# Kernel tuning notes

Hardware: AMD Instinct MI355X
Metric: run time of the kernel (lower is better)

The kernel has to match this reference:

```python
import jax, jax.numpy as jnp
import numpy as np

B, Q, C = 16, 2048, 256
SCORE_THRESH = 0.05   # lowered from 0.7 so the mask is non-trivial with 256 classes
NMS_THRESH = 0.7
LABEL_OFFSET = 1e5    # batched_nms trick: offset boxes per class so cross-class IoU ~ 0


def box_cxcywh_to_xyxy(b):
    cx, cy, w, h = jnp.split(b, 4, axis=-1)
    return jnp.concatenate([cx - 0.5 * w, cy - 0.5 * h, cx + 0.5 * w, cy + 0.5 * h], axis=-1)


def pairwise_iou(boxes):
    # boxes: [N,4] xyxy -> iou: [N,N]
    area = jnp.clip(boxes[:, 2] - boxes[:, 0], 0) * jnp.clip(boxes[:, 3] - boxes[:, 1], 0)
    lt = jnp.maximum(boxes[:, None, :2], boxes[None, :, :2])
    rb = jnp.minimum(boxes[:, None, 2:], boxes[None, :, 2:])
    wh = jnp.clip(rb - lt, 0)
    inter = wh[..., 0] * wh[..., 1]
    union = area[:, None] + area[None, :] - inter
    return inter / jnp.maximum(union, 1e-6)


def nms_single(boxes, scores, labels, valid):
    # Emulates torchvision batched_nms with fixed-size (padded) output:
    # returns score-sorted boxes/scores/labels plus a boolean keep mask.
    n = boxes.shape[0]
    boxes_off = boxes + labels.astype(boxes.dtype)[:, None] * LABEL_OFFSET
    order = jnp.argsort(jnp.where(valid, scores, -jnp.inf))[::-1]
    b_off = boxes_off[order]
    s = scores[order]
    l = labels[order]
    v = valid[order]
    iou = pairwise_iou(b_off)  # [N,N], class-offset so only same-class overlap
    idx = jnp.arange(n)

    def step(keep, x):
        row, i = x  # row: iou of box i vs all
        sup = (row > NMS_THRESH) & (idx > i) & keep[i]
        return keep & ~sup, None

    keep, _ = jax.lax.scan(step, v, (iou, idx))
    return boxes[order], s, l, keep & v


def setup_inputs() -> dict:
    key = jax.random.key(0)
    k1, k2, k3 = jax.random.split(key, 3)
    pred_logits = jax.random.normal(k1, (B, Q, C), dtype=jnp.float32)
    pred_boxes = jax.random.uniform(k2, (B, Q, 4), dtype=jnp.float32)
    target_sizes = jax.random.randint(k3, (B, 2), 480, 1333, dtype=jnp.int32)
    return {"pred_logits": pred_logits, "pred_boxes": pred_boxes, "target_sizes": target_sizes}


def reference(pred_logits, pred_boxes, target_sizes):
    prob = jax.nn.softmax(pred_logits, axis=-1)
    cls_prob = prob[..., :-1]            # drop 'no-object' class
    scores = cls_prob.max(axis=-1)       # [B,Q]
    labels = cls_prob.argmax(axis=-1)    # [B,Q]
    boxes = box_cxcywh_to_xyxy(pred_boxes)
    ts = target_sizes.astype(boxes.dtype)
    img_h, img_w = ts[:, 0], ts[:, 1]
    scale = jnp.stack([img_w, img_h, img_w, img_h], axis=1)  # [B,4]
    boxes = boxes * scale[:, None, :]
    valid = scores >= SCORE_THRESH
    out_boxes, out_scores, out_labels, keep = jax.vmap(nms_single)(boxes, scores, labels, valid)
    return out_boxes, out_scores, out_labels, keep
```

## Files before the change

kernel.cpp:

```cpp
#include <hip/hip_runtime.h>
#include <math.h>

#define NB 16
#define BQ 2048
#define NC 256
#define NL 255

typedef unsigned long long u64;
typedef unsigned int u32;
typedef unsigned short u16;
typedef unsigned char u8;

__device__ __forceinline__ u32 ord_f32(float f) {
  u32 b = __float_as_uint(f);
  return (b & 0x80000000u) ? ~b : (b | 0x80000000u);
}

__global__ __launch_bounds__(256) void score_box_kernel(
    const float* __restrict__ logits,
    const float* __restrict__ pboxes,
    const int* __restrict__ tsz,
    float* __restrict__ out)
{
#pragma clang fp contract(off)
  const int lane = threadIdx.x & 63;
  const int g = lane & 15;
  const int wv = threadIdx.x >> 6;
  const int q = (blockIdx.x * 4 + wv) * 4 + (lane >> 4);
  const float* row = logits + (size_t)q * NC + g * 16;
  const float4 la = *reinterpret_cast<const float4*>(row);
  const float4 lb4 = *reinterpret_cast<const float4*>(row + 4);
  const float4 lc = *reinterpret_cast<const float4*>(row + 8);
  const float4 ld = *reinterpret_cast<const float4*>(row + 12);

  float m = fmaxf(fmaxf(fmaxf(la.x, la.y), fmaxf(la.z, la.w)),
           fmaxf(fmaxf(fmaxf(lb4.x, lb4.y), fmaxf(lb4.z, lb4.w)),
           fmaxf(fmaxf(fmaxf(lc.x, lc.y), fmaxf(lc.z, lc.w)),
                 fmaxf(fmaxf(ld.x, ld.y), fmaxf(ld.z, ld.w)))));
  #pragma unroll
  for (int d = 1; d < 16; d <<= 1) m = fmaxf(m, __shfl_xor(m, d));

  float4 ea, eb, ec, ed;
  ea.x = expf(la.x - m);  ea.y = expf(la.y - m);  ea.z = expf(la.z - m);  ea.w = expf(la.w - m);
  eb.x = expf(lb4.x - m); eb.y = expf(lb4.y - m); eb.z = expf(lb4.z - m); eb.w = expf(lb4.w - m);
  ec.x = expf(lc.x - m);  ec.y = expf(lc.y - m);  ec.z = expf(lc.z - m);  ec.w = expf(lc.w - m);
  ed.x = expf(ld.x - m);  ed.y = expf(ld.y - m);  ed.z = expf(ld.z - m);  ed.w = expf(ld.w - m);

  float s = (((ea.x + ea.y) + (ea.z + ea.w)) + ((eb.x + eb.y) + (eb.z + eb.w)))
          + (((ec.x + ec.y) + (ec.z + ec.w)) + ((ed.x + ed.y) + (ed.z + ed.w)));
  #pragma unroll
  for (int d = 1; d < 16; d <<= 1) s += __shfl_xor(s, d);

  const int c0 = g * 16;
  float bp = ea.x / s; int bc = c0;
  float p;
  p = ea.y / s; if (p > bp) { bp = p; bc = c0 + 1; }
  p = ea.z / s; if (p > bp) { bp = p; bc = c0 + 2; }
  p = ea.w / s; if (p > bp) { bp = p; bc = c0 + 3; }
  p = eb.x / s; if (p > bp) { bp = p; bc = c0 + 4; }
  p = eb.y / s; if (p > bp) { bp = p; bc = c0 + 5; }
  p = eb.z / s; if (p > bp) { bp = p; bc = c0 + 6; }
  p = eb.w / s; if (p > bp) { bp = p; bc = c0 + 7; }
  p = ec.x / s; if (p > bp) { bp = p; bc = c0 + 8; }
  p = ec.y / s; if (p > bp) { bp = p; bc = c0 + 9; }
  p = ec.z / s; if (p > bp) { bp = p; bc = c0 + 10; }
  p = ec.w / s; if (p > bp) { bp = p; bc = c0 + 11; }
  p = ed.x / s; if (p > bp) { bp = p; bc = c0 + 12; }
  p = ed.y / s; if (p > bp) { bp = p; bc = c0 + 13; }
  p = ed.z / s; if (p > bp) { bp = p; bc = c0 + 14; }
  p = ed.w / s; if (g != 15 && p > bp) { bp = p; bc = c0 + 15; }
  #pragma unroll
  for (int d = 1; d < 16; d <<= 1) {
    const float op = __shfl_xor(bp, d);
    const int   oc = __shfl_xor(bc, d);
    if (op > bp || (op == bp && oc < bc)) { bp = op; bc = oc; }
  }

  if (g == 0) {
    const int b = q >> 11;
    float hf = (float)tsz[b * 2 + 0];
    float wf = (float)tsz[b * 2 + 1];
    float4 pb = *reinterpret_cast<const float4*>(pboxes + (size_t)q * 4);
    float hw = 0.5f * pb.z, hh = 0.5f * pb.w;
    float4 ob;
    ob.x = (pb.x - hw) * wf;
    ob.y = (pb.y - hh) * hf;
    ob.z = (pb.x + hw) * wf;
    ob.w = (pb.y + hh) * hf;
    *reinterpret_cast<float4*>(out + (size_t)q * 4) = ob;
    out[NB * BQ * 4 + q] = bp;
    out[NB * BQ * 5 + q] = (float)bc;
  }
}

__global__ __launch_bounds__(1024) void sort_nms_kernel(float* __restrict__ out)
{
#pragma clang fp contract(off)
  __shared__ __align__(16) u64 cvk[BQ];
  __shared__ u32 cgt_a[BQ];
  __shared__ float4 bx[BQ];
  __shared__ float4 bxo[BQ];
  __shared__ u16 gposu[NL * 64];
  __shared__ u8 lbp[BQ];
  __shared__ u8 grank[BQ];
  __shared__ u32 kcnt[256];
  __shared__ u32 wval[16], winv[16];

  const int b = blockIdx.x;
  const int tid = threadIdx.x;
  const int lane = tid & 63;
  const int wv = tid >> 6;
  float* boxes_g  = out + (size_t)b * BQ * 4;
  float* scores_g = out + NB * BQ * 4 + (size_t)b * BQ;
  float* labels_g = out + NB * BQ * 5 + (size_t)b * BQ;
  float* keep_g   = out + NB * BQ * 6 + (size_t)b * BQ;

  const int q0 = 2 * tid;
  float2 s2 = *reinterpret_cast<const float2*>(scores_g + q0);
  float2 lf = *reinterpret_cast<const float2*>(labels_g + q0);
  float4 bb0 = *reinterpret_cast<const float4*>(boxes_g + (size_t)q0 * 4);
  float4 bb1 = *reinterpret_cast<const float4*>(boxes_g + (size_t)q0 * 4 + 4);
  const u32 l0 = (u32)(int)lf.x, l1 = (u32)(int)lf.y;
  bx[q0] = bb0; bx[q0 + 1] = bb1;
  cgt_a[tid] = 0; cgt_a[tid + 1024] = 0;
  if (tid < 256) kcnt[tid] = 0;
  const bool v0 = (s2.x >= 0.05f), v1 = (s2.y >= 0.05f);
  const u64 f0 = ((u64)ord_f32(s2.x) << 32) | ((u32)q0 << 8) | l0;
  const u64 f1 = ((u64)ord_f32(s2.y) << 32) | ((u32)(q0 + 1) << 8) | l1;
  const u64 b0 = __ballot(v0), b1 = __ballot(v1);
  if (lane == 0) {
    const u32 c = (u32)(__popcll(b0) + __popcll(b1));
    wval[wv] = c;
    winv[wv] = 128u - c;
  }
  __syncthreads();

  int nv = 0, voff = 0, ioff = 0;
  #pragma unroll
  for (int w = 0; w < 16; ++w) {
    const int c = (int)wval[w];
    nv += c;
    if (w < wv) { voff += c; ioff += (int)winv[w]; }
  }
  const int tinv = BQ - nv;
  const u64 below = (1ull << lane) - 1ull;
  const int vr0 = voff + (int)__popcll(b0 & below) + (int)__popcll(b1 & below);
  const int ir0 = ioff + (int)__popcll(~b0 & below) + (int)__popcll(~b1 & below);
  const int vr1 = vr0 + (v0 ? 1 : 0);
  const int ir1 = ir0 + (v0 ? 0 : 1);
  if (v0) cvk[vr0] = f0;
  else {
    const int ip = nv + (tinv - 1 - ir0);
    *reinterpret_cast<float4*>(boxes_g + (size_t)ip * 4) = bb0;
    scores_g[ip] = s2.x; labels_g[ip] = lf.x; keep_g[ip] = 0.0f;
  }
  if (v1) cvk[vr1] = f1;
  else {
    const int ip = nv + (tinv - 1 - ir1);
    *reinterpret_cast<float4*>(boxes_g + (size_t)ip * 4) = bb1;
    scores_g[ip] = s2.y; labels_g[ip] = lf.y; keep_g[ip] = 0.0f;
  }
  const int nvc = (nv + 63) >> 6;
  for (int pp = nv + tid; pp < (nvc << 6); pp += 1024) cvk[pp] = 0;
  __syncthreads();

  {
    const int nvS = (nv + 255) >> 8;
    const int nitems = nvS * nvc;
    for (int it = wv; it < nitems; it += 16) {
      const int sc_ = it / nvc;
      const int jc = it - sc_ * nvc;
      const int sb = (sc_ << 8) + lane;
      const u64 ki0 = cvk[sb];
      const u64 ki1 = cvk[sb + 64];
      const u64 ki2 = cvk[sb + 128];
      const u64 ki3 = cvk[sb + 192];
      const ulonglong2* jp2 = reinterpret_cast<const ulonglong2*>(&cvk[jc << 6]);
      u32 c0 = 0, c1 = 0, c2 = 0, c3 = 0;
      #pragma unroll 4
      for (int l2 = 0; l2 < 32; ++l2) {
        const ulonglong2 kj = jp2[l2];
        c0 += ((kj.x > ki0) ? 1u : 0u) + ((kj.y > ki0) ? 1u : 0u);
        c1 += ((kj.x > ki1) ? 1u : 0u) + ((kj.y > ki1) ? 1u : 0u);
        c2 += ((kj.x > ki2) ? 1u : 0u) + ((kj.y > ki2) ? 1u : 0u);
        c3 += ((kj.x > ki3) ? 1u : 0u) + ((kj.y > ki3) ? 1u : 0u);
      }
      if (sb < nv && c0)       atomicAdd(&cgt_a[sb], c0);
      if (sb + 64 < nv && c1)  atomicAdd(&cgt_a[sb + 64], c1);
      if (sb + 128 < nv && c2) atomicAdd(&cgt_a[sb + 128], c2);
      if (sb + 192 < nv && c3) atomicAdd(&cgt_a[sb + 192], c3);
    }
  }
  __syncthreads();

  for (int slot = tid; slot < nv; slot += 1024) {
    const u64 ki = cvk[slot];
    const u32 p = cgt_a[slot];
    const u32 oi = (u32)(ki >> 8) & (BQ - 1);
    const u32 li = (u32)ki & 255u;
    const float4 A = bx[oi];
    *reinterpret_cast<float4*>(boxes_g + (size_t)p * 4) = A;
    scores_g[p] = __uint_as_float((u32)(ki >> 32) & 0x7FFFFFFFu);
    labels_g[p] = (float)li;
    lbp[p] = (u8)li;
    const float lc = (float)li * 100000.0f;
    float4 Ao;
    Ao.x = A.x + lc; Ao.y = A.y + lc; Ao.z = A.z + lc; Ao.w = A.w + lc;
    bxo[p] = Ao;
    const u32 arr = atomicAdd(&kcnt[li], 1u);
    if (arr < 64) gposu[li * 64 + arr] = (u16)p;
  }
  __syncthreads();

  if (tid < NL) {
    const int l = tid;
    int k = (int)kcnt[l]; if (k > 64) k = 64;
    const int base = l * 64;
    for (int a = 1; a < k; ++a) {
      const u16 v = gposu[base + a];
      int e = a;
      while (e > 0 && gposu[base + e - 1] > v) { gposu[base + e] = gposu[base + e - 1]; --e; }
      gposu[base + e] = v;
    }
    if ((int)kcnt[l] <= 64)
      for (int r = 0; r < k; ++r) grank[gposu[base + r]] = (u8)r;
  }
  __syncthreads();

  for (int p = tid; p < nv; p += 1024) {
    const u32 li = lbp[p];
    if (kcnt[li] <= 64) {
      const u32 g = grank[p];
      const u32 st = li * 64;
      const float4 Ao = bxo[p];
      const float areaA = fmaxf(Ao.z - Ao.x, 0.0f) * fmaxf(Ao.w - Ao.y, 0.0f);
      u64 m = 0;
      for (u32 r = 0; r < g; ++r) {
        const int p2 = gposu[st + r];
        const float4 Bo = bxo[p2];
        const float areaB = fmaxf(Bo.z - Bo.x, 0.0f) * fmaxf(Bo.w - Bo.y, 0.0f);
        const float ltx = fmaxf(Ao.x, Bo.x), lty = fmaxf(Ao.y, Bo.y);
        const float rbx = fminf(Ao.z, Bo.z), rby = fminf(Ao.w, Bo.w);
        const float iw = fmaxf(rbx - ltx, 0.0f), ih = fmaxf(rby - lty, 0.0f);
        const float inter = iw * ih;
        const float uni = (areaA + areaB) - inter;
        const float iou = inter / fmaxf(uni, 1e-6f);
        if (iou > 0.7f) m |= (1ull << r);
      }
      cvk[p] = m;
    }
  }
  __syncthreads();

  if (tid < NL) {
    const int l = tid;
    const int k = (int)kcnt[l];
    if (k > 0 && k <= 64) {
      const int st = l * 64;
      u64 kept = 0;
      for (int r = 0; r < k; ++r) {
        const u16 pr = gposu[st + r];
        const u64 m = cvk[pr];
        const int keep = ((m & kept) == 0) ? 1 : 0;
        kept |= (u64)keep << r;
        keep_g[pr] = keep ? 1.0f : 0.0f;
      }
    } else if (k > 64) {
      for (int p2 = 0; p2 < nv; ++p2) {
        if ((int)lbp[p2] != l) continue;
        const float4 Ao = bxo[p2];
        const float areaA = fmaxf(Ao.z - Ao.x, 0.0f) * fmaxf(Ao.w - Ao.y, 0.0f);
        int keep = 1;
        for (int e = 0; e < p2; ++e) {
          if ((int)lbp[e] != l || !grank[e]) continue;
          const float4 Bo = bxo[e];
          const float areaB = fmaxf(Bo.z - Bo.x, 0.0f) * fmaxf(Bo.w - Bo.y, 0.0f);
          const float ltx = fmaxf(Ao.x, Bo.x), lty = fmaxf(Ao.y, Bo.y);
          const float rbx = fminf(Ao.z, Bo.z), rby = fminf(Ao.w, Bo.w);
          const float iw = fmaxf(rbx - ltx, 0.0f), ih = fmaxf(rby - lty, 0.0f);
          const float inter = iw * ih;
          const float uni = (areaA + areaB) - inter;
          const float iou = inter / fmaxf(uni, 1e-6f);
          if (iou > 0.7f) { keep = 0; break; }
        }
        grank[p2] = (u8)keep;
        keep_g[p2] = keep ? 1.0f : 0.0f;
      }
    }
  }
}

extern "C" void kernel_launch(void* const* d_in, const int* in_sizes, int n_in,
                              void* d_out, int out_size, void* d_ws, size_t ws_size,
                              hipStream_t stream) {
  const float* logits = (const float*)d_in[0];
  const float* pboxes = (const float*)d_in[1];
  const int*   tsz    = (const int*)d_in[2];
  float* out = (float*)d_out;
  score_box_kernel<<<NB * BQ / 16, 256, 0, stream>>>(logits, pboxes, tsz, out);
  sort_nms_kernel<<<NB, 1024, 0, stream>>>(out);
}
```

Baseline: 30.66 us.

## Split sort+NMS into compact, multi-block rank, and finish kernels

Splits the single per-image sort/NMS kernel into three launches. A compact kernel writes the valid keys to workspace. A rank kernel then computes counting-sort ranks using 8 blocks per image instead of 16 waves in one block. A finish kernel does the scatter and NMS, staging outputs in shared memory before writing them out coalesced. This spreads the O(n^2) rank work across more CUs, at the cost of two extra launches and global-memory round trips; the rank kernel also reads keys from global memory in a scalar loop.

```diff
diff --git a/kernel.cpp b/kernel.cpp
--- a/kernel.cpp
+++ b/kernel.cpp
@@ -20,7 +20,7 @@
     const float* __restrict__ logits,
     const float* __restrict__ pboxes,
     const int* __restrict__ tsz,
-    float* __restrict__ out)
+    float* __restrict__ ws)
 {
 #pragma clang fp contract(off)
   const int lane = threadIdx.x & 63;
@@ -87,43 +87,39 @@
     ob.y = (pb.y - hh) * hf;
     ob.z = (pb.x + hw) * wf;
     ob.w = (pb.y + hh) * hf;
-    *reinterpret_cast<float4*>(out + (size_t)q * 4) = ob;
-    out[NB * BQ * 4 + q] = bp;
-    out[NB * BQ * 5 + q] = (float)bc;
-  }
-}
-
-__global__ __launch_bounds__(1024) void sort_nms_kernel(float* __restrict__ out)
+    *reinterpret_cast<float4*>(ws + (size_t)q * 4) = ob;
+    ws[NB * BQ * 4 + q] = bp;
+    ws[NB * BQ * 5 + q] = (float)bc;
+  }
+}
+
+__global__ __launch_bounds__(1024) void compact_kernel(
+    const float* __restrict__ ws, float* __restrict__ out,
+    u64* __restrict__ keys_g, u32* __restrict__ nv_g)
 {
-#pragma clang fp contract(off)
   __shared__ __align__(16) u64 cvk[BQ];
-  __shared__ u32 cgt_a[BQ];
-  __shared__ float4 bx[BQ];
-  __shared__ float4 bxo[BQ];
-  __shared__ u16 gposu[NL * 64];
-  __shared__ u8 lbp[BQ];
-  __shared__ u8 grank[BQ];
-  __shared__ u32 kcnt[256];
   __shared__ u32 wval[16], winv[16];
 
   const int b = blockIdx.x;
   const int tid = threadIdx.x;
   const int lane = tid & 63;
   const int wv = tid >> 6;
+  const float* sws = ws + NB * BQ * 4 + (size_t)b * BQ;
+  const float* lws = ws + NB * BQ * 5 + (size_t)b * BQ;
+  const float* bws = ws + (size_t)b * BQ * 4;
   float* boxes_g  = out + (size_t)b * BQ * 4;
   float* scores_g = out + NB * BQ * 4 + (size_t)b * BQ;
   float* labels_g = out + NB * BQ * 5 + (size_t)b * BQ;
   float* keep_g   = out + NB * BQ * 6 + (size_t)b * BQ;
 
   const int q0 = 2 * tid;
-  float2 s2 = *reinterpret_cast<const float2*>(scores_g + q0);
-  float2 lf = *reinterpret_cast<const float2*>(labels_g + q0);
-  float4 bb0 = *reinterpret_cast<const float4*>(boxes_g + (size_t)q0 * 4);
-  float4 bb1 = *reinterpret_cast<const float4*>(boxes_g + (size_t)q0 * 4 + 4);
+  float2 s2 = *reinterpret_cast<const float2*>(sws + q0);
+  float2 lf = *reinterpret_cast<const float2*>(lws + q0);
   const u32 l0 = (u32)(int)lf.x, l1 = (u32)(int)lf.y;
-  bx[q0] = bb0; bx[q0 + 1] = bb1;
-  cgt_a[tid] = 0; cgt_a[tid + 1024] = 0;
-  if (tid < 256) kcnt[tid] = 0;
+  {
+    ulonglong2 z; z.x = 0; z.y = 0;
+    *reinterpret_cast<ulonglong2*>(&cvk[q0]) = z;
+  }
   const bool v0 = (s2.x >= 0.05f), v1 = (s2.y >= 0.05f);
   const u64 f0 = ((u64)ord_f32(s2.x) << 32) | ((u32)q0 << 8) | l0;
   const u64 f1 = ((u64)ord_f32(s2.y) << 32) | ((u32)(q0 + 1) << 8) | l1;
@@ -151,59 +147,92 @@
   if (v0) cvk[vr0] = f0;
   else {
     const int ip = nv + (tinv - 1 - ir0);
-    *reinterpret_cast<float4*>(boxes_g + (size_t)ip * 4) = bb0;
+    *reinterpret_cast<float4*>(boxes_g + (size_t)ip * 4) =
+        *reinterpret_cast<const float4*>(bws + (size_t)q0 * 4);
     scores_g[ip] = s2.x; labels_g[ip] = lf.x; keep_g[ip] = 0.0f;
   }
   if (v1) cvk[vr1] = f1;
   else {
     const int ip = nv + (tinv - 1 - ir1);
-    *reinterpret_cast<float4*>(boxes_g + (size_t)ip * 4) = bb1;
+    *reinterpret_cast<float4*>(boxes_g + (size_t)ip * 4) =
+        *reinterpret_cast<const float4*>(bws + (size_t)q0 * 4 + 4);
     scores_g[ip] = s2.y; labels_g[ip] = lf.y; keep_g[ip] = 0.0f;
   }
-  const int nvc = (nv + 63) >> 6;
-  for (int pp = nv + tid; pp < (nvc << 6); pp += 1024) cvk[pp] = 0;
   __syncthreads();
 
   {
-    const int nvS = (nv + 255) >> 8;
-    const int nitems = nvS * nvc;
-    for (int it = wv; it < nitems; it += 16) {
-      const int sc_ = it / nvc;
-      const int jc = it - sc_ * nvc;
-      const int sb = (sc_ << 8) + lane;
-      const u64 ki0 = cvk[sb];
-      const u64 ki1 = cvk[sb + 64];
-      const u64 ki2 = cvk[sb + 128];
-      const u64 ki3 = cvk[sb + 192];
-      const ulonglong2* jp2 = reinterpret_cast<const ulonglong2*>(&cvk[jc << 6]);
-      u32 c0 = 0, c1 = 0, c2 = 0, c3 = 0;
-      #pragma unroll 4
-      for (int l2 = 0; l2 < 32; ++l2) {
-        const ulonglong2 kj = jp2[l2];
-        c0 += ((kj.x > ki0) ? 1u : 0u) + ((kj.y > ki0) ? 1u : 0u);
-        c1 += ((kj.x > ki1) ? 1u : 0u) + ((kj.y > ki1) ? 1u : 0u);
-        c2 += ((kj.x > ki2) ? 1u : 0u) + ((kj.y > ki2) ? 1u : 0u);
-        c3 += ((kj.x > ki3) ? 1u : 0u) + ((kj.y > ki3) ? 1u : 0u);
-      }
-      if (sb < nv && c0)       atomicAdd(&cgt_a[sb], c0);
-      if (sb + 64 < nv && c1)  atomicAdd(&cgt_a[sb + 64], c1);
-      if (sb + 128 < nv && c2) atomicAdd(&cgt_a[sb + 128], c2);
-      if (sb + 192 < nv && c3) atomicAdd(&cgt_a[sb + 192], c3);
-    }
-  }
+    u64* kb = keys_g + (size_t)b * BQ;
+    *reinterpret_cast<ulonglong2*>(&kb[q0]) =
+        *reinterpret_cast<const ulonglong2*>(&cvk[q0]);
+  }
+  if (tid == 0) nv_g[b] = (u32)nv;
+}
+
+__global__ __launch_bounds__(256) void rank_kernel(
+    const u64* __restrict__ keys_g, const u32* __restrict__ nv_g,
+    u32* __restrict__ rnk_g)
+{
+  const int b = blockIdx.x >> 3;
+  const int slice = blockIdx.x & 7;
+  const int tid = threadIdx.x;
+  const int nv = (int)nv_g[b];
+  const int slot = slice * 256 + tid;
+  if (slice * 256 >= nv) return;
+  const int nvp = (nv + 63) & ~63;
+  const u64* kb = keys_g + (size_t)b * BQ;
+  const u64 ki = kb[slot];
+  u32 c = 0;
+  #pragma unroll 8
+  for (int j = 0; j < nvp; ++j) c += (kb[j] > ki) ? 1u : 0u;
+  if (slot < nv) rnk_g[(size_t)b * BQ + slot] = c;
+}
+
+__global__ __launch_bounds__(1024) void finish_kernel(
+    const float* __restrict__ ws, const u64* __restrict__ keys_g,
+    const u32* __restrict__ nv_g, const u32* __restrict__ rnk_g,
+    float* __restrict__ out)
+{
+#pragma clang fp contract(off)
+  __shared__ __align__(16) u64 cvk[BQ];
+  __shared__ float4 bx[BQ];
+  __shared__ float4 bxo[BQ];
+  __shared__ u16 gposu[NL * 64];
+  __shared__ u16 sidx[BQ];
+  __shared__ u32 sco[BQ];
+  __shared__ u8 lbp[BQ];
+  __shared__ u8 grank[BQ];
+  __shared__ u8 kpf[BQ];
+  __shared__ u32 kcnt[256];
+
+  const int b = blockIdx.x;
+  const int tid = threadIdx.x;
+  const int nv = (int)nv_g[b];
+  const float* bws = ws + (size_t)b * BQ * 4;
+  const u64* kb = keys_g + (size_t)b * BQ;
+  const u32* rb = rnk_g + (size_t)b * BQ;
+  float* boxes_g  = out + (size_t)b * BQ * 4;
+  float* scores_g = out + NB * BQ * 4 + (size_t)b * BQ;
+  float* labels_g = out + NB * BQ * 5 + (size_t)b * BQ;
+  float* keep_g   = out + NB * BQ * 6 + (size_t)b * BQ;
+
+  const int q0 = 2 * tid;
+  *reinterpret_cast<ulonglong2*>(&cvk[q0]) =
+      *reinterpret_cast<const ulonglong2*>(&kb[q0]);
+  bx[q0]     = *reinterpret_cast<const float4*>(bws + (size_t)q0 * 4);
+  bx[q0 + 1] = *reinterpret_cast<const float4*>(bws + (size_t)q0 * 4 + 4);
+  if (tid < 256) kcnt[tid] = 0;
   __syncthreads();
 
   for (int slot = tid; slot < nv; slot += 1024) {
     const u64 ki = cvk[slot];
-    const u32 p = cgt_a[slot];
+    const u32 p = rb[slot];
     const u32 oi = (u32)(ki >> 8) & (BQ - 1);
     const u32 li = (u32)ki & 255u;
+    sidx[p] = (u16)oi;
+    lbp[p] = (u8)li;
+    sco[p] = (u32)(ki >> 32) & 0x7FFFFFFFu;
+    const float lc = (float)li * 100000.0f;
     const float4 A = bx[oi];
-    *reinterpret_cast<float4*>(boxes_g + (size_t)p * 4) = A;
-    scores_g[p] = __uint_as_float((u32)(ki >> 32) & 0x7FFFFFFFu);
-    labels_g[p] = (float)li;
-    lbp[p] = (u8)li;
-    const float lc = (float)li * 100000.0f;
     float4 Ao;
     Ao.x = A.x + lc; Ao.y = A.y + lc; Ao.z = A.z + lc; Ao.w = A.w + lc;
     bxo[p] = Ao;
@@ -263,7 +292,7 @@
         const u64 m = cvk[pr];
         const int keep = ((m & kept) == 0) ? 1 : 0;
         kept |= (u64)keep << r;
-        keep_g[pr] = keep ? 1.0f : 0.0f;
+        kpf[pr] = (u8)keep;
       }
     } else if (k > 64) {
       for (int p2 = 0; p2 < nv; ++p2) {
@@ -284,9 +313,17 @@
           if (iou > 0.7f) { keep = 0; break; }
         }
         grank[p2] = (u8)keep;
-        keep_g[p2] = keep ? 1.0f : 0.0f;
+        kpf[p2] = (u8)keep;
       }
     }
+  }
+  __syncthreads();
+
+  for (int p = tid; p < nv; p += 1024) {
+    *reinterpret_cast<float4*>(boxes_g + (size_t)p * 4) = bx[sidx[p]];
+    scores_g[p] = __uint_as_float(sco[p]);
+    labels_g[p] = (float)lbp[p];
+    keep_g[p]   = kpf[p] ? 1.0f : 0.0f;
   }
 }
 
@@ -297,6 +334,13 @@
   const float* pboxes = (const float*)d_in[1];
   const int*   tsz    = (const int*)d_in[2];
   float* out = (float*)d_out;
-  score_box_kernel<<<NB * BQ / 16, 256, 0, stream>>>(logits, pboxes, tsz, out);
-  sort_nms_kernel<<<NB, 1024, 0, stream>>>(out);
-}
+  float* ws  = (float*)d_ws;
+  char* wsb = (char*)d_ws;
+  u64* keys_g = (u64*)(wsb + (size_t)NB * BQ * 6 * 4);
+  u32* rnk_g  = (u32*)(wsb + (size_t)NB * BQ * 6 * 4 + (size_t)NB * BQ * 8);
+  u32* nv_g   = (u32*)(wsb + (size_t)NB * BQ * 6 * 4 + (size_t)NB * BQ * 8 + (size_t)NB * BQ * 4);
+  score_box_kernel<<<NB * BQ / 16, 256, 0, stream>>>(logits, pboxes, tsz, ws);
+  compact_kernel<<<NB, 1024, 0, stream>>>(ws, out, keys_g, nv_g);
+  rank_kernel<<<NB * 8, 256, 0, stream>>>(keys_g, nv_g, rnk_g);
+  finish_kernel<<<NB, 1024, 0, stream>>>(ws, keys_g, nv_g, rnk_g, out);
+}
```

Result: slower. 51.78 us (+68.9%).

## Split sort/NMS kernel across two blocks per image by label half

Applied to the files above, without the earlier changes.

Launches two blocks per image instead of one. Each block repeats the score sort, then builds per-label groups and runs NMS only for its half of the 255 labels. This halves per-block shared memory for the label tables and spreads the serial per-label NMS work over twice as many CUs, at the cost of doing the rank-counting sort twice. Both blocks read the image's data from the output buffer and write sorted results back into that same buffer with no ordering between blocks, so a block that starts late could read entries the other block has already overwritten.

```diff
diff --git a/kernel.cpp b/kernel.cpp
--- a/kernel.cpp
+++ b/kernel.cpp
@@ -100,13 +100,15 @@
   __shared__ u32 cgt_a[BQ];
   __shared__ float4 bx[BQ];
   __shared__ float4 bxo[BQ];
-  __shared__ u16 gposu[NL * 64];
+  __shared__ u16 gposu[128 * 64];
   __shared__ u8 lbp[BQ];
   __shared__ u8 grank[BQ];
-  __shared__ u32 kcnt[256];
+  __shared__ u32 kcnt[128];
   __shared__ u32 wval[16], winv[16];
 
-  const int b = blockIdx.x;
+  const int b = blockIdx.x >> 1;
+  const int h = blockIdx.x & 1;
+  const u32 labLo = (u32)h * 128u;
   const int tid = threadIdx.x;
   const int lane = tid & 63;
   const int wv = tid >> 6;
@@ -123,7 +125,8 @@
   const u32 l0 = (u32)(int)lf.x, l1 = (u32)(int)lf.y;
   bx[q0] = bb0; bx[q0 + 1] = bb1;
   cgt_a[tid] = 0; cgt_a[tid + 1024] = 0;
-  if (tid < 256) kcnt[tid] = 0;
+  lbp[q0] = 255; lbp[q0 + 1] = 255;
+  if (tid < 128) kcnt[tid] = 0;
   const bool v0 = (s2.x >= 0.05f), v1 = (s2.y >= 0.05f);
   const u64 f0 = ((u64)ord_f32(s2.x) << 32) | ((u32)q0 << 8) | l0;
   const u64 f1 = ((u64)ord_f32(s2.y) << 32) | ((u32)(q0 + 1) << 8) | l1;
@@ -149,13 +152,13 @@
   const int vr1 = vr0 + (v0 ? 1 : 0);
   const int ir1 = ir0 + (v0 ? 0 : 1);
   if (v0) cvk[vr0] = f0;
-  else {
+  else if (h == 0) {
     const int ip = nv + (tinv - 1 - ir0);
     *reinterpret_cast<float4*>(boxes_g + (size_t)ip * 4) = bb0;
     scores_g[ip] = s2.x; labels_g[ip] = lf.x; keep_g[ip] = 0.0f;
   }
   if (v1) cvk[vr1] = f1;
-  else {
+  else if (h == 0) {
     const int ip = nv + (tinv - 1 - ir1);
     *reinterpret_cast<float4*>(boxes_g + (size_t)ip * 4) = bb1;
     scores_g[ip] = s2.y; labels_g[ip] = lf.y; keep_g[ip] = 0.0f;
@@ -195,43 +198,48 @@
 
   for (int slot = tid; slot < nv; slot += 1024) {
     const u64 ki = cvk[slot];
-    const u32 p = cgt_a[slot];
-    const u32 oi = (u32)(ki >> 8) & (BQ - 1);
     const u32 li = (u32)ki & 255u;
-    const float4 A = bx[oi];
-    *reinterpret_cast<float4*>(boxes_g + (size_t)p * 4) = A;
-    scores_g[p] = __uint_as_float((u32)(ki >> 32) & 0x7FFFFFFFu);
-    labels_g[p] = (float)li;
-    lbp[p] = (u8)li;
-    const float lc = (float)li * 100000.0f;
-    float4 Ao;
-    Ao.x = A.x + lc; Ao.y = A.y + lc; Ao.z = A.z + lc; Ao.w = A.w + lc;
-    bxo[p] = Ao;
-    const u32 arr = atomicAdd(&kcnt[li], 1u);
-    if (arr < 64) gposu[li * 64 + arr] = (u16)p;
-  }
-  __syncthreads();
-
-  if (tid < NL) {
-    const int l = tid;
-    int k = (int)kcnt[l]; if (k > 64) k = 64;
-    const int base = l * 64;
+    if ((li - labLo) < 128u) {
+      const u32 p = cgt_a[slot];
+      const u32 oi = (u32)(ki >> 8) & (BQ - 1);
+      const float4 A = bx[oi];
+      *reinterpret_cast<float4*>(boxes_g + (size_t)p * 4) = A;
+      scores_g[p] = __uint_as_float((u32)(ki >> 32) & 0x7FFFFFFFu);
+      labels_g[p] = (float)li;
+      lbp[p] = (u8)li;
+      const float lc = (float)li * 100000.0f;
+      float4 Ao;
+      Ao.x = A.x + lc; Ao.y = A.y + lc; Ao.z = A.z + lc; Ao.w = A.w + lc;
+      bxo[p] = Ao;
+      const u32 ll = li - labLo;
+      const u32 arr = atomicAdd(&kcnt[ll], 1u);
+      if (arr < 64) gposu[ll * 64 + arr] = (u16)p;
+    }
+  }
+  __syncthreads();
+
+  if (tid < 128) {
+    const int ll = tid;
+    int k = (int)kcnt[ll]; if (k > 64) k = 64;
+    const int base = ll * 64;
     for (int a = 1; a < k; ++a) {
       const u16 v = gposu[base + a];
       int e = a;
       while (e > 0 && gposu[base + e - 1] > v) { gposu[base + e] = gposu[base + e - 1]; --e; }
       gposu[base + e] = v;
     }
-    if ((int)kcnt[l] <= 64)
+    if ((int)kcnt[ll] <= 64)
       for (int r = 0; r < k; ++r) grank[gposu[base + r]] = (u8)r;
   }
   __syncthreads();
 
   for (int p = tid; p < nv; p += 1024) {
     const u32 li = lbp[p];
-    if (kcnt[li] <= 64) {
+    if (li == 255u) continue;
+    const u32 ll = li - labLo;
+    if (kcnt[ll] <= 64) {
       const u32 g = grank[p];
-      const u32 st = li * 64;
+      const u32 st = ll * 64;
       const float4 Ao = bxo[p];
       const float areaA = fmaxf(Ao.z - Ao.x, 0.0f) * fmaxf(Ao.w - Ao.y, 0.0f);
       u64 m = 0;
@@ -252,11 +260,12 @@
   }
   __syncthreads();
 
-  if (tid < NL) {
-    const int l = tid;
-    const int k = (int)kcnt[l];
+  if (tid < 128) {
+    const int ll = tid;
+    const int li = (int)labLo + ll;
+    const int k = (int)kcnt[ll];
     if (k > 0 && k <= 64) {
-      const int st = l * 64;
+      const int st = ll * 64;
       u64 kept = 0;
       for (int r = 0; r < k; ++r) {
         const u16 pr = gposu[st + r];
@@ -267,12 +276,12 @@
       }
     } else if (k > 64) {
       for (int p2 = 0; p2 < nv; ++p2) {
-        if ((int)lbp[p2] != l) continue;
+        if ((int)lbp[p2] != li) continue;
         const float4 Ao = bxo[p2];
         const float areaA = fmaxf(Ao.z - Ao.x, 0.0f) * fmaxf(Ao.w - Ao.y, 0.0f);
         int keep = 1;
         for (int e = 0; e < p2; ++e) {
-          if ((int)lbp[e] != l || !grank[e]) continue;
+          if ((int)lbp[e] != li || !grank[e]) continue;
           const float4 Bo = bxo[e];
           const float areaB = fmaxf(Bo.z - Bo.x, 0.0f) * fmaxf(Bo.w - Bo.y, 0.0f);
           const float ltx = fmaxf(Ao.x, Bo.x), lty = fmaxf(Ao.y, Bo.y);
@@ -298,5 +307,5 @@
   const int*   tsz    = (const int*)d_in[2];
   float* out = (float*)d_out;
   score_box_kernel<<<NB * BQ / 16, 256, 0, stream>>>(logits, pboxes, tsz, out);
-  sort_nms_kernel<<<NB, 1024, 0, stream>>>(out);
+  sort_nms_kernel<<<NB * 2, 1024, 0, stream>>>(out);
 }
```

Measured after the change: 31.16 us. About the same (+1.6%).

## Fuse score and NMS kernels into one launch with per-batch flag sync

Applied to the files above, without the earlier changes.

Merges the softmax/box kernel and the sort/NMS kernel into a single launch. The first 512 blocks compute scores into a workspace, and 16 trailing blocks spin on per-batch atomic counters before running NMS. This removes the second kernel launch and lets NMS for early batches overlap with scoring of later ones. In exchange it adds a memset launch, spin-wait cost, dynamic shared memory, and a reduced per-class group cap (32), which routes more classes to the slow fallback path; it also relies on producer blocks being scheduled before the consumers to avoid deadlock.

```diff
diff --git a/kernel.cpp b/kernel.cpp
--- a/kernel.cpp
+++ b/kernel.cpp
@@ -5,6 +5,8 @@
 #define BQ 2048
 #define NC 256
 #define NL 255
+#define ABLK 512
+#define GCAP 32
 
 typedef unsigned long long u64;
 typedef unsigned int u32;
@@ -16,112 +18,127 @@
   return (b & 0x80000000u) ? ~b : (b | 0x80000000u);
 }
 
-__global__ __launch_bounds__(256) void score_box_kernel(
+__global__ __launch_bounds__(1024, 8) void fused_kernel(
     const float* __restrict__ logits,
     const float* __restrict__ pboxes,
     const int* __restrict__ tsz,
+    float* __restrict__ ws,
+    u32* __restrict__ flag,
     float* __restrict__ out)
 {
 #pragma clang fp contract(off)
-  const int lane = threadIdx.x & 63;
-  const int g = lane & 15;
-  const int wv = threadIdx.x >> 6;
-  const int q = (blockIdx.x * 4 + wv) * 4 + (lane >> 4);
-  const float* row = logits + (size_t)q * NC + g * 16;
-  const float4 la = *reinterpret_cast<const float4*>(row);
-  const float4 lb4 = *reinterpret_cast<const float4*>(row + 4);
-  const float4 lc = *reinterpret_cast<const float4*>(row + 8);
-  const float4 ld = *reinterpret_cast<const float4*>(row + 12);
-
-  float m = fmaxf(fmaxf(fmaxf(la.x, la.y), fmaxf(la.z, la.w)),
-           fmaxf(fmaxf(fmaxf(lb4.x, lb4.y), fmaxf(lb4.z, lb4.w)),
-           fmaxf(fmaxf(fmaxf(lc.x, lc.y), fmaxf(lc.z, lc.w)),
-                 fmaxf(fmaxf(ld.x, ld.y), fmaxf(ld.z, ld.w)))));
-  #pragma unroll
-  for (int d = 1; d < 16; d <<= 1) m = fmaxf(m, __shfl_xor(m, d));
-
-  float4 ea, eb, ec, ed;
-  ea.x = expf(la.x - m);  ea.y = expf(la.y - m);  ea.z = expf(la.z - m);  ea.w = expf(la.w - m);
-  eb.x = expf(lb4.x - m); eb.y = expf(lb4.y - m); eb.z = expf(lb4.z - m); eb.w = expf(lb4.w - m);
-  ec.x = expf(lc.x - m);  ec.y = expf(lc.y - m);  ec.z = expf(lc.z - m);  ec.w = expf(lc.w - m);
-  ed.x = expf(ld.x - m);  ed.y = expf(ld.y - m);  ed.z = expf(ld.z - m);  ed.w = expf(ld.w - m);
-
-  float s = (((ea.x + ea.y) + (ea.z + ea.w)) + ((eb.x + eb.y) + (eb.z + eb.w)))
-          + (((ec.x + ec.y) + (ec.z + ec.w)) + ((ed.x + ed.y) + (ed.z + ed.w)));
-  #pragma unroll
-  for (int d = 1; d < 16; d <<= 1) s += __shfl_xor(s, d);
-
-  const int c0 = g * 16;
-  float bp = ea.x / s; int bc = c0;
-  float p;
-  p = ea.y / s; if (p > bp) { bp = p; bc = c0 + 1; }
-  p = ea.z / s; if (p > bp) { bp = p; bc = c0 + 2; }
-  p = ea.w / s; if (p > bp) { bp = p; bc = c0 + 3; }
-  p = eb.x / s; if (p > bp) { bp = p; bc = c0 + 4; }
-  p = eb.y / s; if (p > bp) { bp = p; bc = c0 + 5; }
-  p = eb.z / s; if (p > bp) { bp = p; bc = c0 + 6; }
-  p = eb.w / s; if (p > bp) { bp = p; bc = c0 + 7; }
-  p = ec.x / s; if (p > bp) { bp = p; bc = c0 + 8; }
-  p = ec.y / s; if (p > bp) { bp = p; bc = c0 + 9; }
-  p = ec.z / s; if (p > bp) { bp = p; bc = c0 + 10; }
-  p = ec.w / s; if (p > bp) { bp = p; bc = c0 + 11; }
-  p = ed.x / s; if (p > bp) { bp = p; bc = c0 + 12; }
-  p = ed.y / s; if (p > bp) { bp = p; bc = c0 + 13; }
-  p = ed.z / s; if (p > bp) { bp = p; bc = c0 + 14; }
-  p = ed.w / s; if (g != 15 && p > bp) { bp = p; bc = c0 + 15; }
-  #pragma unroll
-  for (int d = 1; d < 16; d <<= 1) {
-    const float op = __shfl_xor(bp, d);
-    const int   oc = __shfl_xor(bc, d);
-    if (op > bp || (op == bp && oc < bc)) { bp = op; bc = oc; }
-  }
-
-  if (g == 0) {
-    const int b = q >> 11;
-    float hf = (float)tsz[b * 2 + 0];
-    float wf = (float)tsz[b * 2 + 1];
-    float4 pb = *reinterpret_cast<const float4*>(pboxes + (size_t)q * 4);
-    float hw = 0.5f * pb.z, hh = 0.5f * pb.w;
-    float4 ob;
-    ob.x = (pb.x - hw) * wf;
-    ob.y = (pb.y - hh) * hf;
-    ob.z = (pb.x + hw) * wf;
-    ob.w = (pb.y + hh) * hf;
-    *reinterpret_cast<float4*>(out + (size_t)q * 4) = ob;
-    out[NB * BQ * 4 + q] = bp;
-    out[NB * BQ * 5 + q] = (float)bc;
-  }
-}
-
-__global__ __launch_bounds__(1024) void sort_nms_kernel(float* __restrict__ out)
-{
-#pragma clang fp contract(off)
-  __shared__ __align__(16) u64 cvk[BQ];
-  __shared__ u32 cgt_a[BQ];
-  __shared__ float4 bx[BQ];
-  __shared__ float4 bxo[BQ];
-  __shared__ u16 gposu[NL * 64];
-  __shared__ u8 lbp[BQ];
-  __shared__ u8 grank[BQ];
-  __shared__ u32 kcnt[256];
-  __shared__ u32 wval[16], winv[16];
-
-  const int b = blockIdx.x;
+  extern __shared__ __align__(16) char smem[];
   const int tid = threadIdx.x;
   const int lane = tid & 63;
+
+  if (blockIdx.x < ABLK) {
+    const int g = lane & 15;
+    const int wv6 = tid >> 6;
+    const int q = blockIdx.x * 64 + wv6 * 4 + (lane >> 4);
+    const float* row = logits + (size_t)q * NC + g * 16;
+    const float4 la = *reinterpret_cast<const float4*>(row);
+    const float4 lb4 = *reinterpret_cast<const float4*>(row + 4);
+    const float4 lc = *reinterpret_cast<const float4*>(row + 8);
+    const float4 ld = *reinterpret_cast<const float4*>(row + 12);
+
+    float m = fmaxf(fmaxf(fmaxf(la.x, la.y), fmaxf(la.z, la.w)),
+             fmaxf(fmaxf(fmaxf(lb4.x, lb4.y), fmaxf(lb4.z, lb4.w)),
+             fmaxf(fmaxf(fmaxf(lc.x, lc.y), fmaxf(lc.z, lc.w)),
+                   fmaxf(fmaxf(ld.x, ld.y), fmaxf(ld.z, ld.w)))));
+    #pragma unroll
+    for (int d = 1; d < 16; d <<= 1) m = fmaxf(m, __shfl_xor(m, d));
+
+    float4 ea, eb, ec, ed;
+    ea.x = expf(la.x - m);  ea.y = expf(la.y - m);  ea.z = expf(la.z - m);  ea.w = expf(la.w - m);
+    eb.x = expf(lb4.x - m); eb.y = expf(lb4.y - m); eb.z = expf(lb4.z - m); eb.w = expf(lb4.w - m);
+    ec.x = expf(lc.x - m);  ec.y = expf(lc.y - m);  ec.z = expf(lc.z - m);  ec.w = expf(lc.w - m);
+    ed.x = expf(ld.x - m);  ed.y = expf(ld.y - m);  ed.z = expf(ld.z - m);  ed.w = expf(ld.w - m);
+
+    float s = (((ea.x + ea.y) + (ea.z + ea.w)) + ((eb.x + eb.y) + (eb.z + eb.w)))
+            + (((ec.x + ec.y) + (ec.z + ec.w)) + ((ed.x + ed.y) + (ed.z + ed.w)));
+    #pragma unroll
+    for (int d = 1; d < 16; d <<= 1) s += __shfl_xor(s, d);
+
+    const int c0 = g * 16;
+    float bp = ea.x / s; int bc = c0;
+    float p;
+    p = ea.y / s; if (p > bp) { bp = p; bc = c0 + 1; }
+    p = ea.z / s; if (p > bp) { bp = p; bc = c0 + 2; }
+    p = ea.w / s; if (p > bp) { bp = p; bc = c0 + 3; }
+    p = eb.x / s; if (p > bp) { bp = p; bc = c0 + 4; }
+    p = eb.y / s; if (p > bp) { bp = p; bc = c0 + 5; }
+    p = eb.z / s; if (p > bp) { bp = p; bc = c0 + 6; }
+    p = eb.w / s; if (p > bp) { bp = p; bc = c0 + 7; }
+    p = ec.x / s; if (p > bp) { bp = p; bc = c0 + 8; }
+    p = ec.y / s; if (p > bp) { bp = p; bc = c0 + 9; }
+    p = ec.z / s; if (p > bp) { bp = p; bc = c0 + 10; }
+    p = ec.w / s; if (p > bp) { bp = p; bc = c0 + 11; }
+    p = ed.x / s; if (p > bp) { bp = p; bc = c0 + 12; }
+    p = ed.y / s; if (p > bp) { bp = p; bc = c0 + 13; }
+    p = ed.z / s; if (p > bp) { bp = p; bc = c0 + 14; }
+    p = ed.w / s; if (g != 15 && p > bp) { bp = p; bc = c0 + 15; }
+    #pragma unroll
+    for (int d = 1; d < 16; d <<= 1) {
+      const float op = __shfl_xor(bp, d);
+      const int   oc = __shfl_xor(bc, d);
+      if (op > bp || (op == bp && oc < bc)) { bp = op; bc = oc; }
+    }
+
+    if (g == 0) {
+      const int b = q >> 11;
+      float hf = (float)tsz[b * 2 + 0];
+      float wf = (float)tsz[b * 2 + 1];
+      float4 pb = *reinterpret_cast<const float4*>(pboxes + (size_t)q * 4);
+      float hw = 0.5f * pb.z, hh = 0.5f * pb.w;
+      float4 ob;
+      ob.x = (pb.x - hw) * wf;
+      ob.y = (pb.y - hh) * hf;
+      ob.z = (pb.x + hw) * wf;
+      ob.w = (pb.y + hh) * hf;
+      *reinterpret_cast<float4*>(ws + (size_t)q * 4) = ob;
+      ws[NB * BQ * 4 + q] = bp;
+      ws[NB * BQ * 5 + q] = (float)bc;
+    }
+    __syncthreads();
+    if (tid == 0) {
+      __threadfence();
+      atomicAdd(&flag[blockIdx.x >> 5], 1u);
+    }
+    return;
+  }
+
+  const int b = (int)blockIdx.x - ABLK;
+  if (tid == 0) {
+    while (atomicAdd(&flag[b], 0u) < 32u) __builtin_amdgcn_s_sleep(8);
+  }
+  __syncthreads();
+  __threadfence();
+
+  u64*    cvk   = reinterpret_cast<u64*>(smem);
+  float4* bxo   = reinterpret_cast<float4*>(smem + 16384);
+  u32*    cgt_a = reinterpret_cast<u32*>(smem + 49152);
+  u32*    kcnt  = reinterpret_cast<u32*>(smem + 57344);
+  u32*    wval  = reinterpret_cast<u32*>(smem + 58368);
+  u32*    winv  = reinterpret_cast<u32*>(smem + 58432);
+  u16*    gposu = reinterpret_cast<u16*>(smem + 58496);
+  u8*     lbp   = reinterpret_cast<u8*>(smem + 74816);
+  u8*     grank = reinterpret_cast<u8*>(smem + 76864);
+
   const int wv = tid >> 6;
+  const float* bws = ws + (size_t)b * BQ * 4;
+  const float* sws = ws + NB * BQ * 4 + (size_t)b * BQ;
+  const float* lws = ws + NB * BQ * 5 + (size_t)b * BQ;
   float* boxes_g  = out + (size_t)b * BQ * 4;
   float* scores_g = out + NB * BQ * 4 + (size_t)b * BQ;
   float* labels_g = out + NB * BQ * 5 + (size_t)b * BQ;
   float* keep_g   = out + NB * BQ * 6 + (size_t)b * BQ;
 
   const int q0 = 2 * tid;
-  float2 s2 = *reinterpret_cast<const float2*>(scores_g + q0);
-  float2 lf = *reinterpret_cast<const float2*>(labels_g + q0);
-  float4 bb0 = *reinterpret_cast<const float4*>(boxes_g + (size_t)q0 * 4);
-  float4 bb1 = *reinterpret_cast<const float4*>(boxes_g + (size_t)q0 * 4 + 4);
+  float2 s2 = *reinterpret_cast<const float2*>(sws + q0);
+  float2 lf = *reinterpret_cast<const float2*>(lws + q0);
+  float4 bb0 = *reinterpret_cast<const float4*>(bws + (size_t)q0 * 4);
+  float4 bb1 = *reinterpret_cast<const float4*>(bws + (size_t)q0 * 4 + 4);
   const u32 l0 = (u32)(int)lf.x, l1 = (u32)(int)lf.y;
-  bx[q0] = bb0; bx[q0 + 1] = bb1;
   cgt_a[tid] = 0; cgt_a[tid + 1024] = 0;
   if (tid < 256) kcnt[tid] = 0;
   const bool v0 = (s2.x >= 0.05f), v1 = (s2.y >= 0.05f);
@@ -198,7 +215,7 @@
     const u32 p = cgt_a[slot];
     const u32 oi = (u32)(ki >> 8) & (BQ - 1);
     const u32 li = (u32)ki & 255u;
-    const float4 A = bx[oi];
+    const float4 A = *reinterpret_cast<const float4*>(bws + (size_t)oi * 4);
     *reinterpret_cast<float4*>(boxes_g + (size_t)p * 4) = A;
     scores_g[p] = __uint_as_float((u32)(ki >> 32) & 0x7FFFFFFFu);
     labels_g[p] = (float)li;
@@ -208,30 +225,30 @@
     Ao.x = A.x + lc; Ao.y = A.y + lc; Ao.z = A.z + lc; Ao.w = A.w + lc;
     bxo[p] = Ao;
     const u32 arr = atomicAdd(&kcnt[li], 1u);
-    if (arr < 64) gposu[li * 64 + arr] = (u16)p;
+    if (arr < GCAP) gposu[li * GCAP + arr] = (u16)p;
   }
   __syncthreads();
 
   if (tid < NL) {
     const int l = tid;
-    int k = (int)kcnt[l]; if (k > 64) k = 64;
-    const int base = l * 64;
+    int k = (int)kcnt[l]; if (k > GCAP) k = GCAP;
+    const int base = l * GCAP;
     for (int a = 1; a < k; ++a) {
       const u16 v = gposu[base + a];
       int e = a;
       while (e > 0 && gposu[base + e - 1] > v) { gposu[base + e] = gposu[base + e - 1]; --e; }
       gposu[base + e] = v;
     }
-    if ((int)kcnt[l] <= 64)
+    if ((int)kcnt[l] <= GCAP)
       for (int r = 0; r < k; ++r) grank[gposu[base + r]] = (u8)r;
   }
   __syncthreads();
 
   for (int p = tid; p < nv; p += 1024) {
     const u32 li = lbp[p];
-    if (kcnt[li] <= 64) {
+    if (kcnt[li] <= GCAP) {
       const u32 g = grank[p];
-      const u32 st = li * 64;
+      const u32 st = li * GCAP;
       const float4 Ao = bxo[p];
       const float areaA = fmaxf(Ao.z - Ao.x, 0.0f) * fmaxf(Ao.w - Ao.y, 0.0f);
       u64 m = 0;
@@ -255,8 +272,8 @@
   if (tid < NL) {
     const int l = tid;
     const int k = (int)kcnt[l];
-    if (k > 0 && k <= 64) {
-      const int st = l * 64;
+    if (k > 0 && k <= GCAP) {
+      const int st = l * GCAP;
       u64 kept = 0;
       for (int r = 0; r < k; ++r) {
         const u16 pr = gposu[st + r];
@@ -265,7 +282,7 @@
         kept |= (u64)keep << r;
         keep_g[pr] = keep ? 1.0f : 0.0f;
       }
-    } else if (k > 64) {
+    } else if (k > GCAP) {
       for (int p2 = 0; p2 < nv; ++p2) {
         if ((int)lbp[p2] != l) continue;
         const float4 Ao = bxo[p2];
@@ -297,6 +314,8 @@
   const float* pboxes = (const float*)d_in[1];
   const int*   tsz    = (const int*)d_in[2];
   float* out = (float*)d_out;
-  score_box_kernel<<<NB * BQ / 16, 256, 0, stream>>>(logits, pboxes, tsz, out);
-  sort_nms_kernel<<<NB, 1024, 0, stream>>>(out);
+  float* ws  = (float*)d_ws;
+  u32* flag = (u32*)((char*)d_ws + (size_t)NB * BQ * 6 * 4);
+  hipMemsetAsync(flag, 0, NB * sizeof(u32), stream);
+  fused_kernel<<<ABLK + NB, 1024, 78912, 0 ? 0 : stream>>>(logits, pboxes, tsz, ws, flag, out);
 }
```

Result: slower. 50.99 us (+66.3%).
